# Performance work log

Measured on AMD Instinct MI355X. Metric: run time of the kernel, lower is better.

## Reference

```python
import jax, jax.numpy as jnp
import numpy as np

N = 50000
E = 1600000

def setup_inputs() -> dict:
    key = jax.random.key(0)
    ks = jax.random.split(key, 8)
    x = jax.random.normal(ks[0], (N, 512), dtype=jnp.float32)
    edge_index = jax.random.randint(ks[1], (2, E), 0, N, dtype=jnp.int32).astype(jnp.int64)
    eigenvectors = jax.random.normal(ks[2], (N, 128), dtype=jnp.float32)
    W1 = jax.random.normal(ks[3], (512, 128), dtype=jnp.float32) * 0.04
    b1 = jnp.zeros((128,), dtype=jnp.float32)
    W2 = jax.random.normal(ks[4], (128, 64), dtype=jnp.float32) * 0.09
    b2 = jnp.zeros((64,), dtype=jnp.float32)
    lin_W = jax.random.normal(ks[5], (128, 64), dtype=jnp.float32) * 0.09
    W3 = jax.random.normal(ks[6], (128, 40), dtype=jnp.float32) * 0.09
    b3 = jnp.zeros((40,), dtype=jnp.float32)
    return {"x": x, "edge_index": edge_index, "eigenvectors": eigenvectors,
            "W1": W1, "b1": b1, "W2": W2, "b2": b2, "lin_W": lin_W, "W3": W3, "b3": b3}

def _gcn_norm(edge_index, num_nodes):
    # add self loops, then symmetric normalization D^-1/2 (A+I) D^-1/2
    loop = jnp.arange(num_nodes, dtype=edge_index.dtype)
    row = jnp.concatenate([edge_index[0], loop])  # source
    col = jnp.concatenate([edge_index[1], loop])  # target
    w = jnp.ones(row.shape[0], dtype=jnp.float32)
    deg = jax.ops.segment_sum(w, col, num_segments=num_nodes)
    dis = jnp.where(deg > 0, 1.0 / jnp.sqrt(deg), 0.0)
    norm = dis[row] * dis[col]  # [E+N]
    return row, col, norm

def _gcn_conv(h, W, b, row, col, norm, num_nodes):
    h = h @ W                                  # [N, d_out] linear first (PyG order)
    msg = h[row] * norm[:, None]               # gather + scale, [E+N, d_out]
    out = jax.ops.segment_sum(msg, col, num_segments=num_nodes)  # scatter-add
    return out + b

def reference(x, edge_index, eigenvectors, W1, b1, W2, b2, lin_W, W3, b3):
    num_nodes = x.shape[0]
    row, col, norm = _gcn_norm(edge_index, num_nodes)
    h = jax.nn.relu(_gcn_conv(x, W1, b1, row, col, norm, num_nodes))
    # dropout omitted: eval mode (deterministic reference)
    h = jax.nn.relu(_gcn_conv(h, W2, b2, row, col, norm, num_nodes))
    xp = eigenvectors @ lin_W                  # Linear(spec_in, spec_out, bias=False)
    h = jnp.concatenate([h, xp], axis=1)       # [N, h2+spec_out]
    h = _gcn_conv(h, W3, b3, row, col, norm, num_nodes)
    return jax.nn.log_softmax(h, axis=1)
```

## Files before the change

### kernel.cpp

```cpp
#include <hip/hip_runtime.h>
#include <cstdint>
#include <cstddef>

constexpr int BLK = 256;
constexpr int NB = 128;

static inline size_t ws_align(size_t x) { return (x + 255) & ~size_t(255); }

typedef __attribute__((ext_vector_type(8))) short bf16x8;
typedef __attribute__((ext_vector_type(4))) float f32x4;

__device__ inline unsigned short f2bf(float f) {
  unsigned int u = __float_as_uint(f);
  unsigned int r = (u + 0x7fffu + ((u >> 16) & 1u)) >> 16;
  return (unsigned short)r;
}
__device__ inline float bf2f(unsigned short u) {
  return __uint_as_float(((unsigned int)u) << 16);
}
__device__ inline float bf2f_lo(unsigned int w) {
  return __uint_as_float(w << 16);
}
__device__ inline float bf2f_hi(unsigned int w) {
  return __uint_as_float(w & 0xffff0000u);
}

__global__ void k_detect(const int* __restrict__ ei, int* __restrict__ flag) {
  int allz = 1;
  for (int i = 0; i < 32; ++i) allz &= (ei[2 * i + 1] == 0) ? 1 : 0;
  flag[0] = allz;
}

__global__ void k_pack_count(const int* __restrict__ ei, const int* __restrict__ flag,
                             unsigned int* __restrict__ pk,
                             int* __restrict__ cnt, int E, int nChunk) {
  __shared__ int hist[256];
  for (int t = threadIdx.x; t < 256; t += BLK) hist[t] = 0;
  __syncthreads();
  const bool i64 = flag[0] != 0;
  int beg = blockIdx.x * nChunk, end = min(beg + nChunk, E);
  for (int i = beg + threadIdx.x; i < end; i += BLK) {
    int row, col;
    if (i64) { row = ei[2 * i]; col = ei[2 * (E + i)]; }
    else     { row = ei[i];     col = ei[E + i]; }
    unsigned int p = ((unsigned int)col << 16) | (unsigned int)row;
    pk[i] = p;
    atomicAdd(&hist[col >> 8], 1);
  }
  __syncthreads();
  for (int t = threadIdx.x; t < 256; t += BLK) cnt[blockIdx.x * 256 + t] = hist[t];
}

__global__ void k_wscan(const int* __restrict__ cnt, int* __restrict__ woffs,
                        int* __restrict__ base, int nb, int E) {
  __shared__ int wsums[5];
  int w = threadIdx.x;
  int s = 0;
  for (int b = 0; b < nb; ++b) s += cnt[b * 256 + w];
  int lane = w & 63, wv = w >> 6;
  int x = s;
  #pragma unroll
  for (int sh = 1; sh < 64; sh <<= 1) { int t = __shfl_up(x, sh); if (lane >= sh) x += t; }
  if (lane == 63) wsums[wv] = x;
  __syncthreads();
  if (w == 0) { int a = 0; for (int k = 0; k < 4; ++k) { int t = wsums[k]; wsums[k] = a; a += t; } }
  __syncthreads();
  int excl = x - s + wsums[wv];
  woffs[w] = excl;
  if (w == 255) woffs[256] = excl + s;
  int start = excl;
  for (int b = 0; b < nb; ++b) { base[b * 256 + w] = start; start += cnt[b * 256 + w]; }
}

__global__ void k_part_scatter(const unsigned int* __restrict__ pk,
                               const int* __restrict__ base,
                               unsigned int* __restrict__ P, int E, int nChunk) {
  __shared__ int cur[256];
  for (int t = threadIdx.x; t < 256; t += BLK) cur[t] = base[blockIdx.x * 256 + t];
  __syncthreads();
  int beg = blockIdx.x * nChunk, end = min(beg + nChunk, E);
  for (int i = beg + threadIdx.x; i < end; i += BLK) {
    unsigned int p = pk[i];
    int pos = atomicAdd(&cur[p >> 24], 1);
    P[pos] = p;
  }
}

__global__ void k_window_build(const unsigned int* __restrict__ P,
                               const int* __restrict__ woffs,
                               float* __restrict__ dis, int* __restrict__ offs,
                               int* __restrict__ csr, int N, int E) {
  __shared__ int hist[256];
  __shared__ int wsums[5];
  __shared__ int lbase[256];
  const int node0 = blockIdx.x * 256;
  const int t = threadIdx.x;
  hist[t] = 0;
  __syncthreads();
  const int beg = woffs[blockIdx.x], end = woffs[blockIdx.x + 1];
  for (int i = beg + t; i < end; i += BLK)
    atomicAdd(&hist[(P[i] >> 16) & 255], 1);
  __syncthreads();
  const int dg = hist[t];
  if (node0 + t < N) dis[node0 + t] = 1.0f / sqrtf((float)(dg + 1));
  int lane = t & 63, wv = t >> 6;
  int x = dg;
  #pragma unroll
  for (int sh = 1; sh < 64; sh <<= 1) { int q = __shfl_up(x, sh); if (lane >= sh) x += q; }
  if (lane == 63) wsums[wv] = x;
  __syncthreads();
  if (t == 0) { int a = 0; for (int k = 0; k < 4; ++k) { int q = wsums[k]; wsums[k] = a; a += q; } }
  __syncthreads();
  const int goff = beg + (x - dg + wsums[wv]);
  if (node0 + t < N) offs[node0 + t] = goff;
  lbase[t] = goff;
  __syncthreads();
  for (int i = beg + t; i < end; i += BLK) {
    unsigned int p = P[i];
    int pos = atomicAdd(&lbase[(p >> 16) & 255], 1);
    csr[pos] = (int)(p & 0xffffu);
  }
  if (blockIdx.x == 0 && t == 0) offs[N] = E;
}

template<int K, int NOUT, int NOUTP>
__global__ void k_wt(const float* __restrict__ W, unsigned short* __restrict__ WT) {
  int i = blockIdx.x * BLK + threadIdx.x;
  if (i >= NOUTP * K) return;
  int n = i / K, k = i % K;
  float v = (n < NOUT) ? W[(size_t)k * NOUT + n] : 0.f;
  WT[i] = f2bf(v);
}

template<int K, int NT, int MR, bool AF32>
__launch_bounds__(256)
__global__ void k_mgemm(const void* __restrict__ Av, const unsigned short* __restrict__ WT,
                        const float* __restrict__ dis, unsigned short* __restrict__ C,
                        int ldc, int NOUT, int N) {
  const int tid = threadIdx.x;
  const int lane = tid & 63;
  const int wv = tid >> 6;
  const int m = lane & 15;
  const int kq = lane >> 4;
  const int orow = blockIdx.x * (64 * MR) + wv * (16 * MR);

  int rowc[MR];
  #pragma unroll
  for (int mr = 0; mr < MR; ++mr) {
    int row = orow + mr * 16 + m;
    rowc[mr] = row < N ? row : N - 1;
  }

  f32x4 acc[MR][NT];
  #pragma unroll
  for (int mr = 0; mr < MR; ++mr)
    #pragma unroll
    for (int t = 0; t < NT; ++t) acc[mr][t] = {0.f, 0.f, 0.f, 0.f};

  #pragma unroll 2
  for (int k0 = 0; k0 < K; k0 += 32) {
    bf16x8 af[MR];
    #pragma unroll
    for (int mr = 0; mr < MR; ++mr) {
      if constexpr (AF32) {
        const float* Arow = (const float*)Av + (size_t)rowc[mr] * K + kq * 8 + k0;
        float4 a0 = *(const float4*)Arow;
        float4 a1 = *(const float4*)(Arow + 4);
        af[mr][0] = (short)f2bf(a0.x); af[mr][1] = (short)f2bf(a0.y);
        af[mr][2] = (short)f2bf(a0.z); af[mr][3] = (short)f2bf(a0.w);
        af[mr][4] = (short)f2bf(a1.x); af[mr][5] = (short)f2bf(a1.y);
        af[mr][6] = (short)f2bf(a1.z); af[mr][7] = (short)f2bf(a1.w);
      } else {
        const unsigned short* Arow = (const unsigned short*)Av + (size_t)rowc[mr] * K + kq * 8 + k0;
        af[mr] = *(const bf16x8*)Arow;
      }
    }
    bf16x8 bf[NT];
    #pragma unroll
    for (int t = 0; t < NT; ++t)
      bf[t] = *(const bf16x8*)(WT + (size_t)(t * 16 + m) * K + k0 + kq * 8);
    #pragma unroll
    for (int t = 0; t < NT; ++t)
      #pragma unroll
      for (int mr = 0; mr < MR; ++mr)
        acc[mr][t] = __builtin_amdgcn_mfma_f32_16x16x32_bf16(af[mr], bf[t], acc[mr][t], 0, 0, 0);
  }
  #pragma unroll
  for (int mr = 0; mr < MR; ++mr) {
    #pragma unroll
    for (int r = 0; r < 4; ++r) {
      int rr = orow + mr * 16 + kq * 4 + r;
      if (rr < N) {
        float s = dis ? dis[rr] : 1.f;
        #pragma unroll
        for (int t = 0; t < NT; ++t) {
          int cc = t * 16 + m;
          if (cc < NOUT)
            C[(size_t)rr * ldc + cc] = f2bf(acc[mr][t][r] * s);
        }
      }
    }
  }
}

template<int D, bool RELU, bool LOGSM, bool OUTF32>
__launch_bounds__(BLK)
__global__ void k_agg(const unsigned short* __restrict__ g, int ldg,
                      const float* __restrict__ dis, const float* __restrict__ bias,
                      const int* __restrict__ offs, const int* __restrict__ csr,
                      void* __restrict__ dstv, int ldd, int N) {
  int wid = (blockIdx.x * BLK + threadIdx.x) >> 6;
  int lane = threadIdx.x & 63;
  if (wid >= N) return;
  float acc0 = 0.f, acc1 = 0.f;
  if constexpr (D == 128) {
    unsigned int w = *(const unsigned int*)&g[(size_t)wid * ldg + lane * 2];
    acc0 = bf2f_lo(w); acc1 = bf2f_hi(w);
  } else {
    if (lane < D) acc0 = bf2f(g[(size_t)wid * ldg + lane]);
  }
  int beg = offs[wid], end = offs[wid + 1];
  for (int e0 = beg; e0 < end; e0 += 64) {
    int cnt = end - e0; if (cnt > 64) cnt = 64;
    int u = (lane < cnt) ? csr[e0 + lane] : 0;
    int j = 0;
    for (; j + 3 < cnt; j += 4) {
      int u0 = __shfl(u, j), u1 = __shfl(u, j + 1);
      int u2 = __shfl(u, j + 2), u3 = __shfl(u, j + 3);
      if constexpr (D == 128) {
        unsigned int w0 = *(const unsigned int*)&g[(size_t)u0 * ldg + lane * 2];
        unsigned int w1 = *(const unsigned int*)&g[(size_t)u1 * ldg + lane * 2];
        unsigned int w2 = *(const unsigned int*)&g[(size_t)u2 * ldg + lane * 2];
        unsigned int w3 = *(const unsigned int*)&g[(size_t)u3 * ldg + lane * 2];
        acc0 += bf2f_lo(w0) + bf2f_lo(w1) + bf2f_lo(w2) + bf2f_lo(w3);
        acc1 += bf2f_hi(w0) + bf2f_hi(w1) + bf2f_hi(w2) + bf2f_hi(w3);
      } else {
        if (lane < D) {
          float v0 = bf2f(g[(size_t)u0 * ldg + lane]);
          float v1 = bf2f(g[(size_t)u1 * ldg + lane]);
          float v2 = bf2f(g[(size_t)u2 * ldg + lane]);
          float v3 = bf2f(g[(size_t)u3 * ldg + lane]);
          acc0 += (v0 + v1) + (v2 + v3);
        }
      }
    }
    for (; j < cnt; ++j) {
      int u0 = __shfl(u, j);
      if constexpr (D == 128) {
        unsigned int w0 = *(const unsigned int*)&g[(size_t)u0 * ldg + lane * 2];
        acc0 += bf2f_lo(w0); acc1 += bf2f_hi(w0);
      } else {
        if (lane < D) acc0 += bf2f(g[(size_t)u0 * ldg + lane]);
      }
    }
  }
  float dv = dis[wid];
  if constexpr (D == 128) {
    float ox = dv * acc0 + bias[lane * 2];
    float oy = dv * acc1 + bias[lane * 2 + 1];
    if constexpr (RELU) { ox = fmaxf(ox, 0.f); oy = fmaxf(oy, 0.f); }
    unsigned int pw = (unsigned int)f2bf(ox) | ((unsigned int)f2bf(oy) << 16);
    *(unsigned int*)&((unsigned short*)dstv)[(size_t)wid * ldd + lane * 2] = pw;
  } else {
    float o = 0.f;
    if (lane < D) o = dv * acc0 + bias[lane];
    if constexpr (RELU) o = fmaxf(o, 0.f);
    if constexpr (LOGSM) {
      float v = (lane < D) ? o : -__builtin_inff();
      float mx = v;
      #pragma unroll
      for (int s = 32; s >= 1; s >>= 1) mx = fmaxf(mx, __shfl_xor(mx, s));
      float ex = (lane < D) ? expf(v - mx) : 0.f;
      float sum = ex;
      #pragma unroll
      for (int s = 32; s >= 1; s >>= 1) sum += __shfl_xor(sum, s);
      o = v - mx - logf(sum);
    }
    if (lane < D) {
      if constexpr (OUTF32) ((float*)dstv)[(size_t)wid * ldd + lane] = o;
      else ((unsigned short*)dstv)[(size_t)wid * ldd + lane] = f2bf(o);
    }
  }
}

extern "C" void kernel_launch(void* const* d_in, const int* in_sizes, int n_in,
                              void* d_out, int out_size, void* d_ws, size_t ws_size,
                              hipStream_t stream) {
  const float* x    = (const float*)d_in[0];
  const int*   ei   = (const int*)d_in[1];
  const float* eig  = (const float*)d_in[2];
  const float* W1   = (const float*)d_in[3];
  const float* b1   = (const float*)d_in[4];
  const float* W2   = (const float*)d_in[5];
  const float* b2   = (const float*)d_in[6];
  const float* linW = (const float*)d_in[7];
  const float* W3   = (const float*)d_in[8];
  const float* b3   = (const float*)d_in[9];
  float* out = (float*)d_out;

  const int N = in_sizes[0] / 512;
  const int E = in_sizes[1] / 2;

  char* ws = (char*)d_ws;
  size_t off = 0;
  auto alloc = [&](size_t bytes) { char* p = ws + off; off = ws_align(off + bytes); return p; };
  unsigned int* pk = (unsigned int*)alloc((size_t)E * 4);
  unsigned int* P  = (unsigned int*)alloc((size_t)E * 4);
  int*   csr    = (int*)alloc((size_t)E * 4);
  int*   offs   = (int*)alloc((size_t)(N + 1) * 4);
  int*   cnt    = (int*)alloc((size_t)NB * 256 * 4);
  int*   base   = (int*)alloc((size_t)NB * 256 * 4);
  int*   woffs  = (int*)alloc(257 * 4);
  int*   flag   = (int*)alloc(256);
  float* dis    = (float*)alloc((size_t)N * 4);
  unsigned short* F = (unsigned short*)alloc((size_t)N * 128 * 2);
  unsigned short* G = (unsigned short*)alloc((size_t)N * 128 * 2);
  unsigned short* WT1 = (unsigned short*)alloc(128 * 512 * 2);
  unsigned short* WT2 = (unsigned short*)alloc(64 * 128 * 2);
  unsigned short* WTl = (unsigned short*)alloc(64 * 128 * 2);
  unsigned short* WT3 = (unsigned short*)alloc(48 * 128 * 2);

  const int nChunk = (E + NB - 1) / NB;
  const int NW = (N + 255) / 256;

  k_detect<<<1, 1, 0, stream>>>(ei, flag);
  k_pack_count<<<NB, BLK, 0, stream>>>(ei, flag, pk, cnt, E, nChunk);
  k_wscan<<<1, 256, 0, stream>>>(cnt, woffs, base, NB, E);
  k_part_scatter<<<NB, BLK, 0, stream>>>(pk, base, P, E, nChunk);
  k_window_build<<<NW, BLK, 0, stream>>>(P, woffs, dis, offs, csr, N, E);

  k_wt<512, 128, 128><<<(128 * 512 + BLK - 1) / BLK, BLK, 0, stream>>>(W1, WT1);
  k_wt<128, 64, 64><<<(64 * 128 + BLK - 1) / BLK, BLK, 0, stream>>>(W2, WT2);
  k_wt<128, 64, 64><<<(64 * 128 + BLK - 1) / BLK, BLK, 0, stream>>>(linW, WTl);
  k_wt<128, 40, 48><<<(48 * 128 + BLK - 1) / BLK, BLK, 0, stream>>>(W3, WT3);

  const int gG2 = (N + 127) / 128;
  const int gA = (N + 3) / 4;

  k_mgemm<512, 8, 2, true><<<gG2, BLK, 0, stream>>>(x, WT1, dis, F, 128, 128, N);
  k_agg<128, true, false, false><<<gA, BLK, 0, stream>>>(F, 128, dis, b1, offs, csr, G, 128, N);
  k_mgemm<128, 4, 2, false><<<gG2, BLK, 0, stream>>>(G, WT2, dis, F, 64, 64, N);
  k_mgemm<128, 4, 2, true><<<gG2, BLK, 0, stream>>>(eig, WTl, nullptr, G + 64, 128, 64, N);
  k_agg<64, true, false, false><<<gA, BLK, 0, stream>>>(F, 64, dis, b2, offs, csr, G, 128, N);
  k_mgemm<128, 3, 2, false><<<gG2, BLK, 0, stream>>>(G, WT3, dis, F, 40, 40, N);
  k_agg<40, false, true, true><<<gA, BLK, 0, stream>>>(F, 40, dis, b3, offs, csr, out, 40, N);
}
```

Baseline: 334.4 us.

## Add LDS double-buffered first GEMM and half-wave split edge aggregation kernels

Adds a dedicated first-layer GEMM that stages x and the bf16 weights into LDS through direct global-to-LDS loads, double-buffered with an XOR swizzle. The aim is to overlap loads with MFMA and make the uncoalesced per-lane A-row reads coalesced. The aggregation kernels are rewritten so each half-wave handles alternate neighbours with wider per-lane loads, which covers narrow feature widths (64 and 40) without idle lanes. A dedicated 40-wide log-softmax aggregation replaces the general one, and the small GEMM unroll factor goes from 2 to 4. The cost is more code, extra shuffle reductions, and LDS use that may reduce occupancy.

```diff
diff --git a/kernel.cpp b/kernel.cpp
--- a/kernel.cpp
+++ b/kernel.cpp
@@ -23,6 +23,12 @@
 }
 __device__ inline float bf2f_hi(unsigned int w) {
   return __uint_as_float(w & 0xffff0000u);
+}
+
+__device__ inline void gload16(const void* gp, void* lp) {
+  __builtin_amdgcn_global_load_lds(
+      (const __attribute__((address_space(1))) void*)gp,
+      (__attribute__((address_space(3))) void*)lp, 16, 0, 0);
 }
 
 __global__ void k_detect(const int* __restrict__ ei, int* __restrict__ flag) {
@@ -130,6 +136,92 @@
   int n = i / K, k = i % K;
   float v = (n < NOUT) ? W[(size_t)k * NOUT + n] : 0.f;
   WT[i] = f2bf(v);
+}
+
+__global__ __launch_bounds__(256)
+void k_gemm1(const float* __restrict__ x, const unsigned short* __restrict__ WT,
+             const float* __restrict__ dis, unsigned short* __restrict__ C, int N) {
+  __shared__ float As[2][128 * 32];
+  __shared__ unsigned short Wsl[2][4 * 128 * 8];
+  const int tid = threadIdx.x;
+  const int lane = tid & 63, wv = tid >> 6;
+  const int m = lane & 15, kq = lane >> 4;
+  const int row0 = blockIdx.x * 128;
+
+  const int r8 = lane >> 3;
+  const int c8 = lane & 7;
+  int agrow[4];
+  #pragma unroll
+  for (int jj = 0; jj < 4; ++jj) {
+    int gr = row0 + wv * 32 + jj * 8 + r8;
+    agrow[jj] = gr < N ? gr : N - 1;
+  }
+
+  f32x4 acc[2][8];
+  #pragma unroll
+  for (int mr = 0; mr < 2; ++mr)
+    #pragma unroll
+    for (int t = 0; t < 8; ++t) acc[mr][t] = {0.f, 0.f, 0.f, 0.f};
+
+  auto STAGE = [&](int pb, int kb) {
+    #pragma unroll
+    for (int jj = 0; jj < 4; ++jj) {
+      const float* src = x + (size_t)agrow[jj] * 512 + kb * 32 + (c8 ^ r8) * 4;
+      gload16(src, &As[pb][(wv * 32 + jj * 8) * 32]);
+    }
+    #pragma unroll
+    for (int jj = 0; jj < 2; ++jj) {
+      int issue = wv * 2 + jj;
+      int slot = issue >> 1, half = issue & 1;
+      const unsigned short* src = WT + (size_t)(half * 64 + lane) * 512 + kb * 32 + slot * 8;
+      gload16(src, &Wsl[pb][slot * 1024 + half * 512]);
+    }
+  };
+
+  STAGE(0, 0);
+  __syncthreads();
+
+  #pragma unroll 1
+  for (int t = 0; t < 16; ++t) {
+    const int p = t & 1;
+    if (t < 15) STAGE(p ^ 1, t + 1);
+
+    const char* Ab = (const char*)As[p];
+    const char* Wb = (const char*)Wsl[p];
+    bf16x8 af[2];
+    #pragma unroll
+    for (int mr = 0; mr < 2; ++mr) {
+      int row = wv * 32 + mr * 16 + m;
+      int s = row & 7;
+      f32x4 lo = *(const f32x4*)(Ab + row * 128 + ((kq * 2) ^ s) * 16);
+      f32x4 hi = *(const f32x4*)(Ab + row * 128 + ((kq * 2 + 1) ^ s) * 16);
+      af[mr][0] = (short)f2bf(lo[0]); af[mr][1] = (short)f2bf(lo[1]);
+      af[mr][2] = (short)f2bf(lo[2]); af[mr][3] = (short)f2bf(lo[3]);
+      af[mr][4] = (short)f2bf(hi[0]); af[mr][5] = (short)f2bf(hi[1]);
+      af[mr][6] = (short)f2bf(hi[2]); af[mr][7] = (short)f2bf(hi[3]);
+    }
+    #pragma unroll
+    for (int tt = 0; tt < 8; ++tt) {
+      bf16x8 bf = *(const bf16x8*)(Wb + kq * 2048 + (tt * 16 + m) * 16);
+      #pragma unroll
+      for (int mr = 0; mr < 2; ++mr)
+        acc[mr][tt] = __builtin_amdgcn_mfma_f32_16x16x32_bf16(af[mr], bf, acc[mr][tt], 0, 0, 0);
+    }
+    __syncthreads();
+  }
+
+  #pragma unroll
+  for (int mr = 0; mr < 2; ++mr)
+    #pragma unroll
+    for (int r = 0; r < 4; ++r) {
+      int rr = row0 + wv * 32 + mr * 16 + kq * 4 + r;
+      if (rr < N) {
+        float s = dis[rr];
+        #pragma unroll
+        for (int t = 0; t < 8; ++t)
+          C[(size_t)rr * 128 + t * 16 + m] = f2bf(acc[mr][t][r] * s);
+      }
+    }
 }
 
 template<int K, int NT, int MR, bool AF32>
@@ -157,7 +249,7 @@
     #pragma unroll
     for (int t = 0; t < NT; ++t) acc[mr][t] = {0.f, 0.f, 0.f, 0.f};
 
-  #pragma unroll 2
+  #pragma unroll 4
   for (int k0 = 0; k0 < K; k0 += 32) {
     bf16x8 af[MR];
     #pragma unroll
@@ -203,82 +295,124 @@
   }
 }
 
-template<int D, bool RELU, bool LOGSM, bool OUTF32>
+template<int D, bool RELU>
 __launch_bounds__(BLK)
-__global__ void k_agg(const unsigned short* __restrict__ g, int ldg,
-                      const float* __restrict__ dis, const float* __restrict__ bias,
-                      const int* __restrict__ offs, const int* __restrict__ csr,
-                      void* __restrict__ dstv, int ldd, int N) {
+__global__ void k_agg2(const unsigned short* __restrict__ g, int ldg,
+                       const float* __restrict__ dis, const float* __restrict__ bias,
+                       const int* __restrict__ offs, const int* __restrict__ csr,
+                       unsigned short* __restrict__ dst, int ldd, int N) {
+  constexpr int CPL = D / 32;
   int wid = (blockIdx.x * BLK + threadIdx.x) >> 6;
   int lane = threadIdx.x & 63;
   if (wid >= N) return;
-  float acc0 = 0.f, acc1 = 0.f;
-  if constexpr (D == 128) {
-    unsigned int w = *(const unsigned int*)&g[(size_t)wid * ldg + lane * 2];
-    acc0 = bf2f_lo(w); acc1 = bf2f_hi(w);
-  } else {
-    if (lane < D) acc0 = bf2f(g[(size_t)wid * ldg + lane]);
-  }
+  const int l5 = lane >> 5, c = lane & 31;
+  float acc[CPL];
+  #pragma unroll
+  for (int k = 0; k < CPL; ++k) acc[k] = 0.f;
+
+  auto addrow = [&](int r) {
+    if constexpr (CPL == 4) {
+      uint2 w = *(const uint2*)&g[(size_t)r * ldg + c * 4];
+      acc[0] += bf2f_lo(w.x); acc[1] += bf2f_hi(w.x);
+      acc[2] += bf2f_lo(w.y); acc[3] += bf2f_hi(w.y);
+    } else {
+      unsigned int w = *(const unsigned int*)&g[(size_t)r * ldg + c * 2];
+      acc[0] += bf2f_lo(w); acc[1] += bf2f_hi(w);
+    }
+  };
+
+  if (l5 == 0) addrow(wid);
   int beg = offs[wid], end = offs[wid + 1];
   for (int e0 = beg; e0 < end; e0 += 64) {
     int cnt = end - e0; if (cnt > 64) cnt = 64;
     int u = (lane < cnt) ? csr[e0 + lane] : 0;
     int j = 0;
     for (; j + 3 < cnt; j += 4) {
-      int u0 = __shfl(u, j), u1 = __shfl(u, j + 1);
-      int u2 = __shfl(u, j + 2), u3 = __shfl(u, j + 3);
-      if constexpr (D == 128) {
-        unsigned int w0 = *(const unsigned int*)&g[(size_t)u0 * ldg + lane * 2];
-        unsigned int w1 = *(const unsigned int*)&g[(size_t)u1 * ldg + lane * 2];
-        unsigned int w2 = *(const unsigned int*)&g[(size_t)u2 * ldg + lane * 2];
-        unsigned int w3 = *(const unsigned int*)&g[(size_t)u3 * ldg + lane * 2];
-        acc0 += bf2f_lo(w0) + bf2f_lo(w1) + bf2f_lo(w2) + bf2f_lo(w3);
-        acc1 += bf2f_hi(w0) + bf2f_hi(w1) + bf2f_hi(w2) + bf2f_hi(w3);
-      } else {
-        if (lane < D) {
-          float v0 = bf2f(g[(size_t)u0 * ldg + lane]);
-          float v1 = bf2f(g[(size_t)u1 * ldg + lane]);
-          float v2 = bf2f(g[(size_t)u2 * ldg + lane]);
-          float v3 = bf2f(g[(size_t)u3 * ldg + lane]);
-          acc0 += (v0 + v1) + (v2 + v3);
-        }
-      }
-    }
-    for (; j < cnt; ++j) {
-      int u0 = __shfl(u, j);
-      if constexpr (D == 128) {
-        unsigned int w0 = *(const unsigned int*)&g[(size_t)u0 * ldg + lane * 2];
-        acc0 += bf2f_lo(w0); acc1 += bf2f_hi(w0);
-      } else {
-        if (lane < D) acc0 += bf2f(g[(size_t)u0 * ldg + lane]);
-      }
-    }
-  }
-  float dv = dis[wid];
-  if constexpr (D == 128) {
-    float ox = dv * acc0 + bias[lane * 2];
-    float oy = dv * acc1 + bias[lane * 2 + 1];
-    if constexpr (RELU) { ox = fmaxf(ox, 0.f); oy = fmaxf(oy, 0.f); }
-    unsigned int pw = (unsigned int)f2bf(ox) | ((unsigned int)f2bf(oy) << 16);
-    *(unsigned int*)&((unsigned short*)dstv)[(size_t)wid * ldd + lane * 2] = pw;
-  } else {
-    float o = 0.f;
-    if (lane < D) o = dv * acc0 + bias[lane];
-    if constexpr (RELU) o = fmaxf(o, 0.f);
-    if constexpr (LOGSM) {
-      float v = (lane < D) ? o : -__builtin_inff();
-      float mx = v;
-      #pragma unroll
-      for (int s = 32; s >= 1; s >>= 1) mx = fmaxf(mx, __shfl_xor(mx, s));
-      float ex = (lane < D) ? expf(v - mx) : 0.f;
-      float sum = ex;
-      #pragma unroll
-      for (int s = 32; s >= 1; s >>= 1) sum += __shfl_xor(sum, s);
-      o = v - mx - logf(sum);
-    }
-    if (lane < D) {
-      if constexpr (OUTF32) ((float*)dstv)[(size_t)wid * ldd + lane] = o;
-      else ((unsigned short*)dstv)[(size_t)wid * ldd + lane] = f2bf(o);
+      int r0 = __shfl(u, j + l5);
+      int r1 = __shfl(u, j + 2 + l5);
+      addrow(r0); addrow(r1);
+    }
+    for (; j < cnt; j += 2) {
+      int jj = j + l5;
+      int r0 = __shfl(u, jj < cnt ? jj : j);
+      if (jj < cnt) addrow(r0);
+    }
+  }
+  #pragma unroll
+  for (int k = 0; k < CPL; ++k) acc[k] += __shfl_xor(acc[k], 32);
+
+  if (l5 == 0) {
+    float dv = dis[wid];
+    float o[CPL];
+    #pragma unroll
+    for (int k = 0; k < CPL; ++k) {
+      o[k] = dv * acc[k] + bias[c * CPL + k];
+      if constexpr (RELU) o[k] = fmaxf(o[k], 0.f);
+    }
+    if constexpr (CPL == 4) {
+      uint2 pw;
+      pw.x = (unsigned)f2bf(o[0]) | ((unsigned)f2bf(o[1]) << 16);
+      pw.y = (unsigned)f2bf(o[2]) | ((unsigned)f2bf(o[3]) << 16);
+      *(uint2*)&dst[(size_t)wid * ldd + c * 4] = pw;
+    } else {
+      unsigned int pw = (unsigned)f2bf(o[0]) | ((unsigned)f2bf(o[1]) << 16);
+      *(unsigned int*)&dst[(size_t)wid * ldd + c * 2] = pw;
+    }
+  }
+}
+
+__launch_bounds__(BLK)
+__global__ void k_agg40(const unsigned short* __restrict__ g,
+                        const float* __restrict__ dis, const float* __restrict__ bias,
+                        const int* __restrict__ offs, const int* __restrict__ csr,
+                        float* __restrict__ dst, int N) {
+  int wid = (blockIdx.x * BLK + threadIdx.x) >> 6;
+  int lane = threadIdx.x & 63;
+  if (wid >= N) return;
+  const int l5 = lane >> 5, c = lane & 31;
+  const bool act = c < 20;
+  float a0 = 0.f, a1 = 0.f;
+  auto addrow = [&](int r) {
+    if (act) {
+      unsigned int w = *(const unsigned int*)&g[(size_t)r * 40 + c * 2];
+      a0 += bf2f_lo(w); a1 += bf2f_hi(w);
+    }
+  };
+  if (l5 == 0) addrow(wid);
+  int beg = offs[wid], end = offs[wid + 1];
+  for (int e0 = beg; e0 < end; e0 += 64) {
+    int cnt = end - e0; if (cnt > 64) cnt = 64;
+    int u = (lane < cnt) ? csr[e0 + lane] : 0;
+    int j = 0;
+    for (; j + 3 < cnt; j += 4) {
+      int r0 = __shfl(u, j + l5);
+      int r1 = __shfl(u, j + 2 + l5);
+      addrow(r0); addrow(r1);
+    }
+    for (; j < cnt; j += 2) {
+      int jj = j + l5;
+      int r0 = __shfl(u, jj < cnt ? jj : j);
+      if (jj < cnt) addrow(r0);
+    }
+  }
+  a0 += __shfl_xor(a0, 32);
+  a1 += __shfl_xor(a1, 32);
+
+  if (l5 == 0) {
+    float dv = dis[wid];
+    float o0 = act ? dv * a0 + bias[c * 2]     : -__builtin_inff();
+    float o1 = act ? dv * a1 + bias[c * 2 + 1] : -__builtin_inff();
+    float mx = fmaxf(o0, o1);
+    #pragma unroll
+    for (int s = 16; s >= 1; s >>= 1) mx = fmaxf(mx, __shfl_down(mx, s, 32));
+    mx = __shfl(mx, 0, 32);
+    float ex = act ? (expf(o0 - mx) + expf(o1 - mx)) : 0.f;
+    #pragma unroll
+    for (int s = 16; s >= 1; s >>= 1) ex += __shfl_down(ex, s, 32);
+    float ls = logf(__shfl(ex, 0, 32));
+    if (act) {
+      float2 r = make_float2(o0 - mx - ls, o1 - mx - ls);
+      *(float2*)&dst[(size_t)wid * 40 + c * 2] = r;
     }
   }
 }
@@ -334,14 +468,15 @@
   k_wt<128, 64, 64><<<(64 * 128 + BLK - 1) / BLK, BLK, 0, stream>>>(linW, WTl);
   k_wt<128, 40, 48><<<(48 * 128 + BLK - 1) / BLK, BLK, 0, stream>>>(W3, WT3);
 
+  const int gG1 = (N + 127) / 128;
   const int gG2 = (N + 127) / 128;
   const int gA = (N + 3) / 4;
 
-  k_mgemm<512, 8, 2, true><<<gG2, BLK, 0, stream>>>(x, WT1, dis, F, 128, 128, N);
-  k_agg<128, true, false, false><<<gA, BLK, 0, stream>>>(F, 128, dis, b1, offs, csr, G, 128, N);
+  k_gemm1<<<gG1, BLK, 0, stream>>>(x, WT1, dis, F, N);
+  k_agg2<128, true><<<gA, BLK, 0, stream>>>(F, 128, dis, b1, offs, csr, G, 128, N);
   k_mgemm<128, 4, 2, false><<<gG2, BLK, 0, stream>>>(G, WT2, dis, F, 64, 64, N);
   k_mgemm<128, 4, 2, true><<<gG2, BLK, 0, stream>>>(eig, WTl, nullptr, G + 64, 128, 64, N);
-  k_agg<64, true, false, false><<<gA, BLK, 0, stream>>>(F, 64, dis, b2, offs, csr, G, 128, N);
+  k_agg2<64, true><<<gA, BLK, 0, stream>>>(F, 64, dis, b2, offs, csr, G, 128, N);
   k_mgemm<128, 3, 2, false><<<gG2, BLK, 0, stream>>>(G, WT3, dis, F, 40, 40, N);
-  k_agg<40, false, true, true><<<gA, BLK, 0, stream>>>(F, 40, dis, b3, offs, csr, out, 40, N);
-}
+  k_agg40<<<gA, BLK, 0, stream>>>(F, dis, b3, offs, csr, out, N);
+}
```

Measured after the change: 318.1 us. -4.9%, faster.
